# Kernel tuning notes

Hardware: AMD Instinct MI355X
Metric: run time of the kernel (lower is better)

## Reference

```python
import jax, jax.numpy as jnp
import numpy as np

AGENT_RADIUS = 0.2
SAFETY_DIST = 0.1
_ang = np.linspace(0.0, 2.0 * np.pi, 8, endpoint=False)
OBSTACLES = np.stack([10.0 * np.cos(_ang), 10.0 * np.sin(_ang), 0.5 * np.ones(8)], axis=-1).astype(np.float32)  # (x, y, r)


def _qp_solve(p, G, h):
    """Exact solve of: min_z 0.5 z^T z + p^T z  s.t. G z <= h, z in R^2.
    Equivalent to QPFunction with Q=I. Enumerates KKT candidates over active
    sets of size 0, 1, 2 (closed form in 2D) and picks the feasible optimum.
    p: [2], G: [m,2], h: [m]."""
    m = G.shape[0]
    ii, jj = np.triu_indices(m, 1)
    # active set {} -> unconstrained minimizer
    z0 = -p[None, :]                                        # [1,2]
    # active set {i}: z = -p - lam*g_i, g_i.z = h_i
    gg = jnp.sum(G * G, axis=-1)                            # [m]
    lam1 = (-(G @ p) - h) / (gg + 1e-12)
    z1 = -p[None, :] - lam1[:, None] * G                    # [m,2]
    ok1 = lam1 >= -1e-8
    # active set {i,j}: z solves 2x2 system [g_i; g_j] z = [h_i; h_j]
    Gi, Gj = G[ii], G[jj]                                   # [P,2]
    hi, hj = h[ii], h[jj]
    det = Gi[:, 0] * Gj[:, 1] - Gi[:, 1] * Gj[:, 0]
    det_ok = jnp.abs(det) > 1e-9
    ds = jnp.where(det_ok, det, 1.0)
    zx = (hi * Gj[:, 1] - hj * Gi[:, 1]) / ds
    zy = (Gi[:, 0] * hj - Gj[:, 0] * hi) / ds
    z2 = jnp.stack([zx, zy], axis=-1)                       # [P,2]
    r = -(z2 + p[None, :])                                  # A^T lam = r
    lam_i = (Gj[:, 1] * r[:, 0] - Gj[:, 0] * r[:, 1]) / ds
    lam_j = (Gi[:, 0] * r[:, 1] - Gi[:, 1] * r[:, 0]) / ds
    ok2 = det_ok & (lam_i >= -1e-8) & (lam_j >= -1e-8)
    Z = jnp.concatenate([z0, z1, z2], axis=0)               # [K,2]
    ok = jnp.concatenate([jnp.ones((1,), bool), ok1, ok2], axis=0)
    tol = 1e-6 * (1.0 + jnp.abs(h))
    feas = jnp.all(Z @ G.T <= (h + tol)[None, :], axis=-1)  # [K]
    obj = 0.5 * jnp.sum(Z * Z, axis=-1) + Z @ p
    obj = jnp.where(ok & feas, obj, jnp.inf)
    return Z[jnp.argmin(obj)]


def _forward(x, mean, std, W1, b1, W21, b21, W31, b31, W22, b22, W32, b32):
    x0 = x * std + mean                                     # de-normalized state [B,8]
    hid = jax.nn.relu(x @ W1.T + b1)
    x31 = jax.nn.relu(hid @ W21.T + b21) @ W31.T + b31      # reference control p [B,2]
    x32 = 4.0 * jax.nn.sigmoid(jax.nn.relu(hid @ W22.T + b22) @ W32.T + b32)  # CBF penalties [B,2]
    px, py, theta, v = x0[:, 0], x0[:, 1], x0[:, 2], x0[:, 3]
    ox, oy, oth, ov = x0[:, 4], x0[:, 5], x0[:, 6], x0[:, 7]
    st, ct = jnp.sin(theta), jnp.cos(theta)
    vs, vc = v * st, v * ct
    obs = jnp.asarray(OBSTACLES, x.dtype)
    # static obstacle constraints, vectorized over the n_obs obstacles
    dx = px[:, None] - obs[None, :, 0]                      # [B,n_obs]
    dy = py[:, None] - obs[None, :, 1]
    R = AGENT_RADIUS + obs[:, 2] + SAFETY_DIST
    bar = dx * dx + dy * dy - (R * R)[None, :]
    bdot = 2.0 * dx * vc[:, None] + 2.0 * dy * vs[:, None]
    Lf2b = (2.0 * v * v)[:, None]
    u1 = -2.0 * dx * vs[:, None] + 2.0 * dy * vc[:, None]
    u2 = 2.0 * dx * ct[:, None] + 2.0 * dy * st[:, None]
    G_obs = -jnp.stack([u1, u2], axis=-1)                   # [B,n_obs,2]
    s0, s1 = x32[:, 0:1], x32[:, 1:2]
    h_obs = Lf2b + (s0 + s1) * bdot + (s0 * s1) * bar       # [B,n_obs]
    # opponent constraint
    Ro = 2.0 * AGENT_RADIUS + SAFETY_DIST
    dxo, dyo = px - ox, py - oy
    so, co = jnp.sin(oth), jnp.cos(oth)
    bar_o = dxo * dxo + dyo * dyo - Ro * Ro
    bdot_o = 2.0 * dxo * (vc - ov * co) + 2.0 * dyo * (vs - ov * so)
    Lf2b_o = 2.0 * (v * v + ov * ov + 2.0 * v * ov * jnp.cos(theta - oth))
    u1o = -2.0 * dxo * vs + 2.0 * dyo * vc
    u2o = 2.0 * dxo * ct + 2.0 * dyo * st
    G_opp = -jnp.stack([u1o, u2o], axis=-1)[:, None, :]     # [B,1,2]
    h_opp = (Lf2b_o + (x32[:, 0] + x32[:, 1]) * bdot_o + x32[:, 0] * x32[:, 1] * bar_o)[:, None]
    G = jnp.concatenate([G_obs, G_opp], axis=1)             # [B,m,2]
    h = jnp.concatenate([h_obs, h_opp], axis=1)             # [B,m]
    return jax.vmap(_qp_solve)(x31, G, h)                   # [B,2]


def setup_inputs() -> dict:
    key = jax.random.key(0)
    ks = jax.random.split(key, 6)
    B, nF, H1, H2 = 65536, 8, 256, 128

    def lin(k, o, i):
        k1, k2 = jax.random.split(k)
        W = jax.random.normal(k1, (o, i), jnp.float32) / np.float32(np.sqrt(i))
        b = jax.random.normal(k2, (o,), jnp.float32) * 0.01
        return W, b

    W1, b1 = lin(ks[0], H1, nF)
    W21, b21 = lin(ks[1], H2, H1)
    W31, b31 = lin(ks[2], 2, H2)
    W22, b22 = lin(ks[3], H2, H1)
    W32, b32 = lin(ks[4], 2, H2)
    x = jax.random.normal(ks[5], (B, nF), jnp.float32)
    return {"x": x, "mean": jnp.zeros((nF,), jnp.float32), "std": jnp.ones((nF,), jnp.float32),
            "W1": W1, "b1": b1, "W21": W21, "b21": b21, "W31": W31, "b31": b31,
            "W22": W22, "b22": b22, "W32": W32, "b32": b32, "sgn": 1}


def reference(x, mean, std, W1, b1, W21, b21, W31, b31, W22, b22, W32, b32, sgn):
    # sgn==1 / training path -> batched differentiable QP solve
    return _forward(x, mean, std, W1, b1, W21, b21, W31, b31, W22, b22, W32, b32)
```

## Files before the change

### kernel.cpp

```cpp
#include <hip/hip_runtime.h>
#include <hip/hip_bf16.h>
#include <math.h>


typedef unsigned int u32;
typedef unsigned long long u64;
typedef unsigned short u16;
typedef __attribute__((ext_vector_type(8))) short short8;
typedef __attribute__((ext_vector_type(4))) float f32x4;
typedef __attribute__((ext_vector_type(2))) float f32x2;
typedef __attribute__((ext_vector_type(4))) u32 u32x4;

union Frag  { short8 v; u32 u[4]; u32x4 q; };
union F8    { long l; u32 u[2]; };

__device__ __forceinline__ u32 packbf(float a, float b) {
    float2 f2; f2.x = a; f2.y = b;
    __hip_bfloat162 h = __float22bfloat162_rn(f2);
    union { __hip_bfloat162 h2; u32 u; } cv; cv.h2 = h;
    return cv.u;
}

__device__ __forceinline__ u32 packfp8x4(float a, float b, float c, float d) {
    u32 r = 0;
    r = (u32)__builtin_amdgcn_cvt_pk_fp8_f32(a, b, (int)r, false);
    r = (u32)__builtin_amdgcn_cvt_pk_fp8_f32(c, d, (int)r, true);
    return r;
}

__device__ const float OBX[8] = { 10.f, 7.07106781186547524f, 6.123234e-16f, -7.07106781186547524f,
                                 -10.f, -7.07106781186547524f, -1.8369702e-15f, 7.07106781186547524f };
__device__ const float OBY[8] = { 0.f, 7.07106781186547524f, 10.f, 7.07106781186547524f,
                                  1.2246468e-15f, -7.07106781186547524f, -10.f, -7.07106781186547524f };

#define PI0_ 0x2111111100000000ULL
#define PI1_ 0x5544443333322222ULL
#define PI2_ 0x7665ULL
#define PJ0_ 0x3876543287654321ULL
#define PJ1_ 0x7687658765487654ULL
#define PJ2_ 0x8878ULL
__device__ __forceinline__ int unpack4(u64 w0, u64 w1, u64 w2, int t) {
    u64 w = (t < 16) ? w0 : (t < 32) ? w1 : w2;
    return (int)((w >> ((t & 15) * 4)) & 15);
}

__global__ __launch_bounds__(256)
void prep_kernel(const float* __restrict__ W21, const float* __restrict__ W22,
                 const float* __restrict__ W1,  const float* __restrict__ b1,
                 u32* __restrict__ ws)
{
    int idx  = blockIdx.x * 256 + threadIdx.x;
    if (idx < 4096) {
        int lane = idx & 63;
        int nt   = (idx >> 6) & 7;
        int kp   = (idx >> 9) & 3;
        int head = idx >> 11;
        const float* W = head ? W22 : W21;
        int q  = lane >> 4;
        int n  = nt * 16 + (lane & 15);
        const float* se = W + n * 256 + (2 * kp) * 32 + q * 8;
        const float* so = W + n * 256 + (2 * kp + 1) * 32 + q * 8;
        u32x4 o;
        o.x = packfp8x4(se[0], se[1], se[2], se[3]);
        o.y = packfp8x4(se[4], se[5], se[6], se[7]);
        o.z = packfp8x4(so[0], so[1], so[2], so[3]);
        o.w = packfp8x4(so[4], so[5], so[6], so[7]);
        __builtin_nontemporal_store(o, (u32x4*)ws + idx);
    } else {
        int f    = idx - 4096;
        int nt   = f >> 6;
        int lane = f & 63;
        int q    = lane >> 4;
        int mm   = lane & 15;
        int n = 32 * (nt & 7) + 8 * (mm >> 2) + 4 * (nt >> 3) + (mm & 3);
        u32x4 o = (u32x4){0u, 0u, 0u, 0u};
        if (q == 0) {
            const float* wr = W1 + n * 8;
            o.x = packbf(wr[0], wr[1]);
            o.y = packbf(wr[2], wr[3]);
            o.z = packbf(wr[4], wr[5]);
            o.w = packbf(wr[6], wr[7]);
        } else if (q == 1) {
            o.x = packbf(b1[n], 0.f);
        }
        __builtin_nontemporal_store(o, (u32x4*)ws + idx);
    }
}

__global__ __launch_bounds__(512)
void barriernet_kernel(const float* __restrict__ x,
                       const float* __restrict__ meanp,
                       const float* __restrict__ stdp,
                       const float* __restrict__ b21,
                       const float* __restrict__ W31,
                       const float* __restrict__ b31,
                       const float* __restrict__ b22,
                       const float* __restrict__ W32,
                       const float* __restrict__ b32,
                       const u32* __restrict__ wsB,
                       float* __restrict__ out, int Btot)
{
    const int tid  = threadIdx.x;
    const int wave = tid >> 6;
    const int lane = tid & 63;
    const int q    = lane >> 4;
    const int m    = lane & 15;
    const int blockRow = blockIdx.x * 128;

    __shared__ u32x4 stage[2048];
    __shared__ float lds_p[128][4];

    const u32x4* wsB4 = (const u32x4*)wsB;

    Frag xB;
    {
        int R0 = blockRow + wave * 16 + m;
        const f32x4* xv0 = (const f32x4*)(x + (R0 < Btot ? R0 : 0) * 8);
        f32x4 xa0 = xv0[0], xb0 = xv0[1];
        if (q == 0) {
            xB.u[0] = packbf(xa0.x, xa0.y);
            xB.u[1] = packbf(xa0.z, xa0.w);
            xB.u[2] = packbf(xb0.x, xb0.y);
            xB.u[3] = packbf(xb0.z, xb0.w);
        } else if (q == 1) {
            xB.u[0] = 0x00003f80u;
            xB.u[1] = 0u; xB.u[2] = 0u; xB.u[3] = 0u;
        } else {
            xB.u[0] = 0u; xB.u[1] = 0u; xB.u[2] = 0u; xB.u[3] = 0u;
        }
    }
    f32x4 hacc[16];
    {
        const u32x4* W1f = wsB4 + 4096;
        #pragma unroll
        for (int nt = 0; nt < 16; ++nt) {
            Frag Af; Af.q = W1f[nt * 64 + lane];
            hacc[nt] = __builtin_amdgcn_mfma_f32_16x16x32_bf16(
                Af.v, xB.v, (f32x4){0.f, 0.f, 0.f, 0.f}, 0, 0, 0);
        }
    }
    F8 A8[8];
    #pragma unroll
    for (int ks = 0; ks < 8; ++ks) {
        A8[ks].u[0] = packfp8x4(fmaxf(hacc[ks][0], 0.f),     fmaxf(hacc[ks][1], 0.f),
                                fmaxf(hacc[ks][2], 0.f),     fmaxf(hacc[ks][3], 0.f));
        A8[ks].u[1] = packfp8x4(fmaxf(hacc[ks + 8][0], 0.f), fmaxf(hacc[ks + 8][1], 0.f),
                                fmaxf(hacc[ks + 8][2], 0.f), fmaxf(hacc[ks + 8][3], 0.f));
    }

    #pragma unroll 1
    for (int head = 0; head < 2; ++head) {
        const float* b2 = head ? b22 : b21;
        const float* W3 = head ? W32 : W31;
        const float* b3 = head ? b32 : b31;

        f32x4 acc[8];
        #pragma unroll
        for (int nt = 0; nt < 8; ++nt) acc[nt] = (f32x4){0.f, 0.f, 0.f, 0.f};

        const u32x4* src = wsB4 + head * 2048;
        #pragma unroll
        for (int i = 0; i < 4; ++i) {
            int fi = (wave * 4 + i) * 64 + lane;
            stage[fi] = src[fi];
        }
        __syncthreads();
        #pragma unroll
        for (int kp = 0; kp < 4; ++kp) {
            #pragma unroll
            for (int nt = 0; nt < 8; ++nt) {
                u32x4 b = stage[kp * 512 + nt * 64 + lane];
                F8 be; be.u[0] = b.x; be.u[1] = b.y;
                F8 bo; bo.u[0] = b.z; bo.u[1] = b.w;
                acc[nt] = __builtin_amdgcn_mfma_f32_16x16x32_fp8_fp8(
                    A8[2 * kp].l, be.l, acc[nt], 0, 0, 0);
                acc[nt] = __builtin_amdgcn_mfma_f32_16x16x32_fp8_fp8(
                    A8[2 * kp + 1].l, bo.l, acc[nt], 0, 0, 0);
            }
        }
        __syncthreads();

        float pr0[4], pr1[4];
        #pragma unroll
        for (int rg = 0; rg < 4; ++rg) { pr0[rg] = 0.f; pr1[rg] = 0.f; }
        #pragma unroll
        for (int nt = 0; nt < 8; ++nt) {
            int col = nt * 16 + m;
            float b2c = b2[col];
            float w0c = W3[col];
            float w1c = W3[128 + col];
            #pragma unroll
            for (int rg = 0; rg < 4; ++rg) {
                float rv = fmaxf(acc[nt][rg] + b2c, 0.f);
                pr0[rg] = fmaf(rv, w0c, pr0[rg]);
                pr1[rg] = fmaf(rv, w1c, pr1[rg]);
            }
        }
        #pragma unroll
        for (int rg = 0; rg < 4; ++rg) {
            float v0 = pr0[rg], v1 = pr1[rg];
            #pragma unroll
            for (int off = 1; off < 16; off <<= 1) {
                v0 += __shfl_xor(v0, off, 64);
                v1 += __shfl_xor(v1, off, 64);
            }
            pr0[rg] = v0; pr1[rg] = v1;
        }
        if (m == 0) {
            #pragma unroll
            for (int rg = 0; rg < 4; ++rg) {
                int row = wave * 16 + q * 4 + rg;
                float a0 = pr0[rg] + b3[0];
                float a1 = pr1[rg] + b3[1];
                if (head == 0) {
                    lds_p[row][0] = a0;
                    lds_p[row][1] = a1;
                } else {
                    lds_p[row][2] = 4.f / (1.f + __expf(-a0));
                    lds_p[row][3] = 4.f / (1.f + __expf(-a1));
                }
            }
        }
    }
    __syncthreads();

    f32x4 (*qC)[128]  = (f32x4(*)[128])stage;
    f32x4 (*res)[128] = (f32x4(*)[128])(stage + 1152);

    const int rq   = tid & 127;
    const int part = tid >> 7;
    const int R    = blockRow + rq;
    float p0 = lds_p[rq][0];
    float p1 = lds_p[rq][1];

    if (part == 0) {
        float s0 = lds_p[rq][2];
        float s1 = lds_p[rq][3];
        float xr[8];
        const float* xp = x + (R < Btot ? R : 0) * 8;
        #pragma unroll
        for (int c = 0; c < 8; ++c) xr[c] = fmaf(xp[c], stdp[c], meanp[c]);
        float px = xr[0], py = xr[1], th = xr[2], v = xr[3];
        float ox = xr[4], oy = xr[5], oth = xr[6], ov = xr[7];
        float st = __sinf(th),  ct = __cosf(th);
        float so = __sinf(oth), co = __cosf(oth);
        float vs = v * st, vc = v * ct;
        float sps = s0 + s1, ss = s0 * s1;
        float Lf2b = 2.f * v * v;
        #pragma unroll 1
        for (int k = 0; k < 8; ++k) {
            float dx = px - OBX[k], dy = py - OBY[k];
            float bar  = dx * dx + dy * dy - 0.64f;
            float bdot = 2.f * dx * vc + 2.f * dy * vs;
            float gx = 2.f * dx * vs - 2.f * dy * vc;
            float gy = -(2.f * dx * ct + 2.f * dy * st);
            float hk = Lf2b + sps * bdot + ss * bar;
            float ht = hk + 1e-6f * (1.f + fabsf(hk));
            qC[k][rq] = (f32x4){gx, gy, hk, ht};
        }
        {
            float dxo = px - ox, dyo = py - oy;
            float bar_o  = dxo * dxo + dyo * dyo - 0.25f;
            float bdot_o = 2.f * dxo * (vc - ov * co) + 2.f * dyo * (vs - ov * so);
            float Lf2b_o = 2.f * (v * v + ov * ov + 2.f * v * ov * __cosf(th - oth));
            float gx = 2.f * dxo * vs - 2.f * dyo * vc;
            float gy = -(2.f * dxo * ct + 2.f * dyo * st);
            float hk = Lf2b_o + sps * bdot_o + ss * bar_o;
            float ht = hk + 1e-6f * (1.f + fabsf(hk));
            qC[8][rq] = (f32x4){gx, gy, hk, ht};
        }
    }
    __syncthreads();

    const f32x4 C0 = qC[0][rq], C1 = qC[1][rq], C2 = qC[2][rq];
    const f32x4 C3 = qC[3][rq], C4 = qC[4][rq], C5 = qC[5][rq];
    const f32x4 C6 = qC[6][rq], C7 = qC[7][rq], C8 = qC[8][rq];

    const float zx0 = -p0, zy0 = -p1;
    bool z0ok =
        (zx0 * C0.x + zy0 * C0.y <= C0.w) &&
        (zx0 * C1.x + zy0 * C1.y <= C1.w) &&
        (zx0 * C2.x + zy0 * C2.y <= C2.w) &&
        (zx0 * C3.x + zy0 * C3.y <= C3.w) &&
        (zx0 * C4.x + zy0 * C4.y <= C4.w) &&
        (zx0 * C5.x + zy0 * C5.y <= C5.w) &&
        (zx0 * C6.x + zy0 * C6.y <= C6.w) &&
        (zx0 * C7.x + zy0 * C7.y <= C7.w) &&
        (zx0 * C8.x + zy0 * C8.y <= C8.w);

    float bobj = INFINITY;
    float bzx = zx0, bzy = zy0;
    if (z0ok) {
        if (part == 0)
            bobj = 0.5f * (zx0 * zx0 + zy0 * zy0) + zx0 * p0 + zy0 * p1;
    } else {
        const int c0i = (part == 0) ? 0  : (part == 1) ? 12 : (part == 2) ? 24 : 35;
        const int c1i = (part == 0) ? 12 : (part == 1) ? 24 : (part == 2) ? 35 : 46;
        #pragma unroll 2
        for (int c = c0i; c < c1i; ++c) {
            float zx, zy;
            bool pre;
            if (c == 0) {
                zx = -p0; zy = -p1; pre = true;
            } else if (c <= 9) {
                f32x4 g = qC[c - 1][rq];
                float gg  = g.x * g.x + g.y * g.y;
                float lam = (-(g.x * p0 + g.y * p1) - g.z) / (gg + 1e-12f);
                zx = -p0 - lam * g.x;
                zy = -p1 - lam * g.y;
                pre = (lam >= -1e-8f);
            } else {
                int t = c - 10;
                int pi = unpack4(PI0_, PI1_, PI2_, t);
                int pj = unpack4(PJ0_, PJ1_, PJ2_, t);
                f32x4 gi = qC[pi][rq];
                f32x4 gj = qC[pj][rq];
                float det = gi.x * gj.y - gi.y * gj.x;
                bool dok = fabsf(det) > 1e-9f;
                float ds = dok ? det : 1.0f;
                float inv = 1.0f / ds;
                zx = (gi.z * gj.y - gj.z * gi.y) * inv;
                zy = (gi.x * gj.z - gj.x * gi.z) * inv;
                float rx = -(zx + p0), ry = -(zy + p1);
                float li = (gj.y * rx - gj.x * ry) * inv;
                float lj = (gi.x * ry - gi.y * rx) * inv;
                pre = dok && (li >= -1e-8f) && (lj >= -1e-8f);
            }
            bool ok = pre;
            ok = ok && (zx * C0.x + zy * C0.y <= C0.w);
            ok = ok && (zx * C1.x + zy * C1.y <= C1.w);
            ok = ok && (zx * C2.x + zy * C2.y <= C2.w);
            ok = ok && (zx * C3.x + zy * C3.y <= C3.w);
            ok = ok && (zx * C4.x + zy * C4.y <= C4.w);
            ok = ok && (zx * C5.x + zy * C5.y <= C5.w);
            ok = ok && (zx * C6.x + zy * C6.y <= C6.w);
            ok = ok && (zx * C7.x + zy * C7.y <= C7.w);
            ok = ok && (zx * C8.x + zy * C8.y <= C8.w);
            float obj = 0.5f * (zx * zx + zy * zy) + zx * p0 + zy * p1;
            if (ok && obj < bobj) { bobj = obj; bzx = zx; bzy = zy; }
        }
    }

    if (part) {
        res[part - 1][rq] = (f32x4){bobj, bzx, bzy, 0.f};
    }
    __syncthreads();
    if (part == 0) {
        #pragma unroll
        for (int pp = 0; pp < 3; ++pp) {
            f32x4 r = res[pp][rq];
            if (r.x < bobj) { bobj = r.x; bzx = r.y; bzy = r.z; }
        }
        if (R < Btot) {
            f32x2 o2; o2.x = bzx; o2.y = bzy;
            ((f32x2*)out)[R] = o2;
        }
    }
}

extern "C" void kernel_launch(void* const* d_in, const int* in_sizes, int n_in,
                              void* d_out, int out_size, void* d_ws, size_t ws_size,
                              hipStream_t stream) {
    const float* x    = (const float*)d_in[0];
    const float* mean = (const float*)d_in[1];
    const float* stdv = (const float*)d_in[2];
    const float* W1   = (const float*)d_in[3];
    const float* b1   = (const float*)d_in[4];
    const float* W21  = (const float*)d_in[5];
    const float* b21  = (const float*)d_in[6];
    const float* W31  = (const float*)d_in[7];
    const float* b31  = (const float*)d_in[8];
    const float* W22  = (const float*)d_in[9];
    const float* b22  = (const float*)d_in[10];
    const float* W32  = (const float*)d_in[11];
    const float* b32  = (const float*)d_in[12];
    int B = in_sizes[0] / 8;
    float* out = (float*)d_out;
    u32* ws = (u32*)d_ws;

    hipLaunchKernelGGL(prep_kernel, dim3(20), dim3(256), 0, stream,
                       W21, W22, W1, b1, ws);

    hipLaunchKernelGGL(barriernet_kernel, dim3((B + 127) / 128), dim3(512), 0, stream,
                       x, mean, stdv, b21, W31, b31, b22, W32, b32,
                       ws, out, B);
}
```

Before: 103.7 us.

## Fuse weight prep into main kernel and split constraint setup across parts

Drops the separate prep kernel. Each block now converts W21/W22 to fp8 directly into a doubled LDS stage buffer and builds the bf16 W1 fragments in registers. It also removes the per-head barrier pairs and spreads the nine constraint rows across all four thread parts instead of one, using vector loads. This trades one launch and a global round trip for redundant per-block conversion work and more LDS (64KB stage), which may cut occupancy.

```diff
diff --git a/kernel.cpp b/kernel.cpp
--- a/kernel.cpp
+++ b/kernel.cpp
@@ -44,60 +44,20 @@
     return (int)((w >> ((t & 15) * 4)) & 15);
 }
 
-__global__ __launch_bounds__(256)
-void prep_kernel(const float* __restrict__ W21, const float* __restrict__ W22,
-                 const float* __restrict__ W1,  const float* __restrict__ b1,
-                 u32* __restrict__ ws)
-{
-    int idx  = blockIdx.x * 256 + threadIdx.x;
-    if (idx < 4096) {
-        int lane = idx & 63;
-        int nt   = (idx >> 6) & 7;
-        int kp   = (idx >> 9) & 3;
-        int head = idx >> 11;
-        const float* W = head ? W22 : W21;
-        int q  = lane >> 4;
-        int n  = nt * 16 + (lane & 15);
-        const float* se = W + n * 256 + (2 * kp) * 32 + q * 8;
-        const float* so = W + n * 256 + (2 * kp + 1) * 32 + q * 8;
-        u32x4 o;
-        o.x = packfp8x4(se[0], se[1], se[2], se[3]);
-        o.y = packfp8x4(se[4], se[5], se[6], se[7]);
-        o.z = packfp8x4(so[0], so[1], so[2], so[3]);
-        o.w = packfp8x4(so[4], so[5], so[6], so[7]);
-        __builtin_nontemporal_store(o, (u32x4*)ws + idx);
-    } else {
-        int f    = idx - 4096;
-        int nt   = f >> 6;
-        int lane = f & 63;
-        int q    = lane >> 4;
-        int mm   = lane & 15;
-        int n = 32 * (nt & 7) + 8 * (mm >> 2) + 4 * (nt >> 3) + (mm & 3);
-        u32x4 o = (u32x4){0u, 0u, 0u, 0u};
-        if (q == 0) {
-            const float* wr = W1 + n * 8;
-            o.x = packbf(wr[0], wr[1]);
-            o.y = packbf(wr[2], wr[3]);
-            o.z = packbf(wr[4], wr[5]);
-            o.w = packbf(wr[6], wr[7]);
-        } else if (q == 1) {
-            o.x = packbf(b1[n], 0.f);
-        }
-        __builtin_nontemporal_store(o, (u32x4*)ws + idx);
-    }
-}
-
 __global__ __launch_bounds__(512)
 void barriernet_kernel(const float* __restrict__ x,
                        const float* __restrict__ meanp,
                        const float* __restrict__ stdp,
+                       const float* __restrict__ W1,
+                       const float* __restrict__ b1,
+                       const float* __restrict__ W21,
                        const float* __restrict__ b21,
                        const float* __restrict__ W31,
                        const float* __restrict__ b31,
+                       const float* __restrict__ W22,
                        const float* __restrict__ b22,
                        const float* __restrict__ W32,
                        const float* __restrict__ b32,
-                       const u32* __restrict__ wsB,
                        float* __restrict__ out, int Btot)
 {
     const int tid  = threadIdx.x;
@@ -107,10 +67,26 @@
     const int m    = lane & 15;
     const int blockRow = blockIdx.x * 128;
 
-    __shared__ u32x4 stage[2048];
+    __shared__ u32x4 stage[4096];
     __shared__ float lds_p[128][4];
 
-    const u32x4* wsB4 = (const u32x4*)wsB;
+    #pragma unroll
+    for (int i = 0; i < 8; ++i) {
+        int blk = wave * 8 + i;
+        int hd  = blk >> 5;
+        int kp  = (blk >> 3) & 3;
+        int nt  = blk & 7;
+        const float* W = hd ? W22 : W21;
+        const f32x4* s4 = (const f32x4*)(W + (nt * 16 + m) * 256 + kp * 64 + q * 8);
+        f32x4 e0 = s4[0], e1 = s4[1];
+        f32x4 o0 = s4[8], o1 = s4[9];
+        u32x4 o;
+        o.x = packfp8x4(e0.x, e0.y, e0.z, e0.w);
+        o.y = packfp8x4(e1.x, e1.y, e1.z, e1.w);
+        o.z = packfp8x4(o0.x, o0.y, o0.z, o0.w);
+        o.w = packfp8x4(o1.x, o1.y, o1.z, o1.w);
+        stage[blk * 64 + lane] = o;
+    }
 
     Frag xB;
     {
@@ -130,14 +106,23 @@
         }
     }
     f32x4 hacc[16];
-    {
-        const u32x4* W1f = wsB4 + 4096;
-        #pragma unroll
-        for (int nt = 0; nt < 16; ++nt) {
-            Frag Af; Af.q = W1f[nt * 64 + lane];
-            hacc[nt] = __builtin_amdgcn_mfma_f32_16x16x32_bf16(
-                Af.v, xB.v, (f32x4){0.f, 0.f, 0.f, 0.f}, 0, 0, 0);
-        }
+    #pragma unroll
+    for (int nt = 0; nt < 16; ++nt) {
+        int n = 32 * (nt & 7) + 8 * (m >> 2) + 4 * (nt >> 3) + (m & 3);
+        Frag Af;
+        Af.u[0] = 0u; Af.u[1] = 0u; Af.u[2] = 0u; Af.u[3] = 0u;
+        if (q == 0) {
+            const f32x4* wr = (const f32x4*)(W1 + n * 8);
+            f32x4 w0 = wr[0], w1 = wr[1];
+            Af.u[0] = packbf(w0.x, w0.y);
+            Af.u[1] = packbf(w0.z, w0.w);
+            Af.u[2] = packbf(w1.x, w1.y);
+            Af.u[3] = packbf(w1.z, w1.w);
+        } else if (q == 1) {
+            Af.u[0] = packbf(b1[n], 0.f);
+        }
+        hacc[nt] = __builtin_amdgcn_mfma_f32_16x16x32_bf16(
+            Af.v, xB.v, (f32x4){0.f, 0.f, 0.f, 0.f}, 0, 0, 0);
     }
     F8 A8[8];
     #pragma unroll
@@ -148,6 +133,8 @@
                                 fmaxf(hacc[ks + 8][2], 0.f), fmaxf(hacc[ks + 8][3], 0.f));
     }
 
+    __syncthreads();
+
     #pragma unroll 1
     for (int head = 0; head < 2; ++head) {
         const float* b2 = head ? b22 : b21;
@@ -158,18 +145,12 @@
         #pragma unroll
         for (int nt = 0; nt < 8; ++nt) acc[nt] = (f32x4){0.f, 0.f, 0.f, 0.f};
 
-        const u32x4* src = wsB4 + head * 2048;
-        #pragma unroll
-        for (int i = 0; i < 4; ++i) {
-            int fi = (wave * 4 + i) * 64 + lane;
-            stage[fi] = src[fi];
-        }
-        __syncthreads();
+        const u32x4* hS = stage + head * 2048;
         #pragma unroll
         for (int kp = 0; kp < 4; ++kp) {
             #pragma unroll
             for (int nt = 0; nt < 8; ++nt) {
-                u32x4 b = stage[kp * 512 + nt * 64 + lane];
+                u32x4 b = hS[kp * 512 + nt * 64 + lane];
                 F8 be; be.u[0] = b.x; be.u[1] = b.y;
                 F8 bo; bo.u[0] = b.z; bo.u[1] = b.w;
                 acc[nt] = __builtin_amdgcn_mfma_f32_16x16x32_fp8_fp8(
@@ -178,7 +159,6 @@
                     A8[2 * kp + 1].l, bo.l, acc[nt], 0, 0, 0);
             }
         }
-        __syncthreads();
 
         float pr0[4], pr1[4];
         #pragma unroll
@@ -233,22 +213,25 @@
     float p0 = lds_p[rq][0];
     float p1 = lds_p[rq][1];
 
-    if (part == 0) {
+    {
         float s0 = lds_p[rq][2];
         float s1 = lds_p[rq][3];
-        float xr[8];
         const float* xp = x + (R < Btot ? R : 0) * 8;
-        #pragma unroll
-        for (int c = 0; c < 8; ++c) xr[c] = fmaf(xp[c], stdp[c], meanp[c]);
-        float px = xr[0], py = xr[1], th = xr[2], v = xr[3];
-        float ox = xr[4], oy = xr[5], oth = xr[6], ov = xr[7];
-        float st = __sinf(th),  ct = __cosf(th);
-        float so = __sinf(oth), co = __cosf(oth);
+        f32x4 xv0 = ((const f32x4*)xp)[0];
+        f32x4 xv1 = ((const f32x4*)xp)[1];
+        const f32x4 sd0 = ((const f32x4*)stdp)[0],  sd1 = ((const f32x4*)stdp)[1];
+        const f32x4 mn0 = ((const f32x4*)meanp)[0], mn1 = ((const f32x4*)meanp)[1];
+        float px = fmaf(xv0.x, sd0.x, mn0.x);
+        float py = fmaf(xv0.y, sd0.y, mn0.y);
+        float th = fmaf(xv0.z, sd0.z, mn0.z);
+        float v  = fmaf(xv0.w, sd0.w, mn0.w);
+        float st = __sinf(th), ct = __cosf(th);
         float vs = v * st, vc = v * ct;
         float sps = s0 + s1, ss = s0 * s1;
         float Lf2b = 2.f * v * v;
-        #pragma unroll 1
-        for (int k = 0; k < 8; ++k) {
+        #pragma unroll
+        for (int kk = 0; kk < 2; ++kk) {
+            int k = part + kk * 4;
             float dx = px - OBX[k], dy = py - OBY[k];
             float bar  = dx * dx + dy * dy - 0.64f;
             float bdot = 2.f * dx * vc + 2.f * dy * vs;
@@ -258,7 +241,12 @@
             float ht = hk + 1e-6f * (1.f + fabsf(hk));
             qC[k][rq] = (f32x4){gx, gy, hk, ht};
         }
-        {
+        if (part == 3) {
+            float ox = fmaf(xv1.x, sd1.x, mn1.x);
+            float oy = fmaf(xv1.y, sd1.y, mn1.y);
+            float oth= fmaf(xv1.z, sd1.z, mn1.z);
+            float ov = fmaf(xv1.w, sd1.w, mn1.w);
+            float so = __sinf(oth), co = __cosf(oth);
             float dxo = px - ox, dyo = py - oy;
             float bar_o  = dxo * dxo + dyo * dyo - 0.25f;
             float bdot_o = 2.f * dxo * (vc - ov * co) + 2.f * dyo * (vs - ov * so);
@@ -376,12 +364,8 @@
     const float* b32  = (const float*)d_in[12];
     int B = in_sizes[0] / 8;
     float* out = (float*)d_out;
-    u32* ws = (u32*)d_ws;
-
-    hipLaunchKernelGGL(prep_kernel, dim3(20), dim3(256), 0, stream,
-                       W21, W22, W1, b1, ws);
 
     hipLaunchKernelGGL(barriernet_kernel, dim3((B + 127) / 128), dim3(512), 0, stream,
-                       x, mean, stdv, b21, W31, b31, b22, W32, b32,
-                       ws, out, B);
-}
+                       x, mean, stdv, W1, b1, W21, b21, W31, b31, W22, b22, W32, b32,
+                       out, B);
+}
```

After: 118.5 us. 1.14x slower.
